# Optimization experiments

Hardware: AMD Instinct MI355X
Metric: run time of the kernel (lower is better)

Reference implementation:

```python
import jax, jax.numpy as jnp
import numpy as np

VOCAB_SIZE = 250002
UNUSED_TOKEN_IDS = np.array([0, 2, 1, 3])  # cls, eos, pad, unk (XLM-R tokenizer)
EPS = 1e-12


def _l2norm(x):
    n = jnp.sqrt(jnp.sum(x * x, axis=-1, keepdims=True))
    return x / jnp.maximum(n, EPS)


def setup_inputs() -> dict:
    key = jax.random.key(0)
    k1, k2, k3, k4 = jax.random.split(key, 4)
    B, S, H = 16, 2048, 1024
    hidden_state = jax.random.normal(k1, (B, S, H), dtype=jnp.float32)
    attention_mask = jnp.ones((B, S), dtype=jnp.float32)
    input_ids = jax.random.randint(k2, (B, S), 0, VOCAB_SIZE, dtype=jnp.int64)
    sparse_W = jax.random.normal(k3, (H, 1), dtype=jnp.float32) * 0.02
    sparse_b = jnp.zeros((1,), dtype=jnp.float32)
    colbert_W = jax.random.normal(k4, (H, H), dtype=jnp.float32) * 0.02
    colbert_b = jnp.zeros((H,), dtype=jnp.float32)
    return {
        "hidden_state": hidden_state,
        "attention_mask": attention_mask,
        "input_ids": input_ids,
        "sparse_W": sparse_W,
        "sparse_b": sparse_b,
        "colbert_W": colbert_W,
        "colbert_b": colbert_b,
    }


def reference(hidden_state, attention_mask, input_ids, sparse_W, sparse_b, colbert_W, colbert_b):
    B, S, H = hidden_state.shape
    # dense vector: CLS token, L2-normalized
    dense_vecs = _l2norm(hidden_state[:, 0])  # (B, H)

    # sparse: relu(Linear(H,1)) per token, scatter into vocab, max over seq.
    # scatter into zeros(B,S,V) + max over dim=1 == per-batch scatter-max into (B,V)
    token_weights = jax.nn.relu(
        jnp.einsum("bsh,ho->bso", hidden_state, sparse_W) + sparse_b
    )[..., 0]  # (B, S)
    batch_idx = jnp.arange(B)[:, None]  # (B, 1)
    sparse_vecs = jnp.zeros((B, VOCAB_SIZE), dtype=token_weights.dtype)
    sparse_vecs = sparse_vecs.at[batch_idx, input_ids].max(token_weights)
    # zero out special tokens (cls/eos/pad/unk)
    sparse_vecs = sparse_vecs.at[:, jnp.asarray(UNUSED_TOKEN_IDS)].set(0.0)

    # colbert: Linear(H,H) on tokens 1:, masked, then L2-normalized
    colbert_vecs = jnp.einsum("bsh,hd->bsd", hidden_state[:, 1:], colbert_W) + colbert_b
    colbert_vecs = colbert_vecs * attention_mask[:, 1:, None]
    colbert_vecs = _l2norm(colbert_vecs)  # (B, S-1, H)

    return dense_vecs, sparse_vecs, colbert_vecs
```

## Files before the change

kernel.cpp:

```cpp
#include <hip/hip_runtime.h>

#define HDIM 1024
#define SEQ  2048
#define BATCH 16
#define VOCAB 250002
#define M_TOT (BATCH * SEQ)
#define SPARSE_OFF (BATCH * HDIM)
#define COLBERT_OFF (SPARSE_OFF + BATCH * VOCAB)

typedef __attribute__((ext_vector_type(8))) short short8;
typedef __attribute__((ext_vector_type(4))) float f32x4;

static __device__ __forceinline__ unsigned short f2bf(float f) {
  union { float f; unsigned u; } v; v.f = f;
  unsigned r = v.u + 0x7fffu + ((v.u >> 16) & 1u);
  return (unsigned short)(r >> 16);
}

__global__ __launch_bounds__(256) void prep_kernel(
    const float* __restrict__ W, unsigned short* __restrict__ Wt,
    float* __restrict__ out, const float* __restrict__ hidden)
{
  __shared__ float tile[32][33];
  __shared__ float red[4];
  const int blk = blockIdx.x;
  if (blk < 1024) {
    const int n0 = (blk & 31) * 32, k0 = (blk >> 5) * 32;
    const int tx = threadIdx.x & 31, ty = threadIdx.x >> 5;
#pragma unroll
    for (int i = ty; i < 32; i += 8)
      tile[i][tx] = W[(size_t)(k0 + i) * HDIM + n0 + tx];
    __syncthreads();
#pragma unroll
    for (int i = ty; i < 32; i += 8) {
      const int n = n0 + i, k = k0 + tx;
      const size_t idx = (size_t)((n >> 4) * 32 + (k >> 5)) * 512
                       + (size_t)((((k >> 3) & 3) * 16 + (n & 15)) * 8 + (k & 7));
      Wt[idx] = f2bf(tile[tx][i]);
    }
  } else if (blk < 1536) {
    float4 z = {0.f, 0.f, 0.f, 0.f};
    float4* p = (float4*)(out + SPARSE_OFF);
    int idx = (blk - 1024) * 256 + threadIdx.x;
#pragma unroll 1
    for (; idx < 1000008; idx += 512 * 256) p[idx] = z;
  } else {
    const int b = blk - 1536;
    const int t = threadIdx.x;
    const float4* x = (const float4*)(hidden + (size_t)b * SEQ * HDIM);
    float4 v = x[t];
    float ss = v.x * v.x + v.y * v.y + v.z * v.z + v.w * v.w;
#pragma unroll
    for (int off = 32; off; off >>= 1) ss += __shfl_down(ss, off);
    if ((t & 63) == 0) red[t >> 6] = ss;
    __syncthreads();
    float tot = red[0] + red[1] + red[2] + red[3];
    float inv = 1.0f / fmaxf(sqrtf(tot), 1e-12f);
    v.x *= inv; v.y *= inv; v.z *= inv; v.w *= inv;
    ((float4*)(out + (size_t)b * HDIM))[t] = v;
  }
}

#define FUSED_LDS (64 * HDIM * 2 + (64 * 8 + 64) * 4)

__global__ __launch_bounds__(512, 2) void fused_kernel(
    const float* __restrict__ hidden,
    const unsigned short* __restrict__ Bp,
    const float* __restrict__ bias,
    const float* __restrict__ mask,
    const float* __restrict__ sparse_W,
    const float* __restrict__ sparse_b,
    const int* __restrict__ input_ids,
    float* __restrict__ out)
{
  extern __shared__ __align__(16) char smem[];
  unsigned short* As = (unsigned short*)smem;
  float* redLDS = (float*)(smem + 64 * HDIM * 2);
  float* invLDS = redLDS + 64 * 8;

  const int t = threadIdx.x;
  const int w = t >> 6, l = t & 63;
  const int q = l >> 4, ml = l & 15;
  const int mBase = blockIdx.x * 64;

  {
    const float sb = sparse_b[0];
    for (int r8 = 0; r8 < 8; r8++) {
      const int row = w * 8 + r8;
      const int gm = mBase + row;
      const float* src = hidden + (size_t)gm * HDIM;
      float dot = 0.f;
#pragma unroll
      for (int c = 0; c < 2; c++) {
        const int k0 = c * 512 + l * 8;
        f32x4 x0 = __builtin_nontemporal_load((const f32x4*)(src + k0));
        f32x4 x1 = __builtin_nontemporal_load((const f32x4*)(src + k0) + 1);
        const f32x4 w0 = *((const f32x4*)(sparse_W + k0));
        const f32x4 w1 = *((const f32x4*)(sparse_W + k0) + 1);
        dot = fmaf(x0.x, w0.x, dot); dot = fmaf(x0.y, w0.y, dot);
        dot = fmaf(x0.z, w0.z, dot); dot = fmaf(x0.w, w0.w, dot);
        dot = fmaf(x1.x, w1.x, dot); dot = fmaf(x1.y, w1.y, dot);
        dot = fmaf(x1.z, w1.z, dot); dot = fmaf(x1.w, w1.w, dot);
        short8 o;
        o[0] = (short)f2bf(x0.x); o[1] = (short)f2bf(x0.y);
        o[2] = (short)f2bf(x0.z); o[3] = (short)f2bf(x0.w);
        o[4] = (short)f2bf(x1.x); o[5] = (short)f2bf(x1.y);
        o[6] = (short)f2bf(x1.z); o[7] = (short)f2bf(x1.w);
        const int kk = k0 >> 5;
        const int slot = (((k0 >> 3) & 3) + (row >> 1)) & 3;
        const int byte = (kk * 4096 + row * 64 + slot * 16) ^ ((kk & 1) << 6);
        *(short8*)(smem + byte) = o;
      }
#pragma unroll
      for (int off = 32; off; off >>= 1) dot += __shfl_down(dot, off);
      if (l == 0) {
        const float wgt = dot + sb;
        if (wgt > 0.f) {
          const int id = input_ids[gm];
          if (id > 3) {
            const int b = gm >> 11;
            atomicMax((int*)(out + SPARSE_OFF + (size_t)b * VOCAB + id),
                      __float_as_int(wgt));
          }
        }
      }
    }
  }
  __syncthreads();

  int aoff[4];
#pragma unroll
  for (int i = 0; i < 4; i++) {
    const int ar = i * 16 + ml;
    aoff[i] = ar * 64 + (((q + (ar >> 1)) & 3) * 16);
  }
  const unsigned short* Bpw = Bp + (size_t)(w * 8 * 32) * 512 + l * 8;

  f32x4 acc[4][8] = {};
  short8 aC[4], aN[4], b0[4], b1[4];

#define LOADA(dst, KK) do {                                              \
    const int fl_ = ((KK) & 1) << 6;                                     \
    const int kb_ = (KK) * 4096;                                         \
    _Pragma("unroll")                                                    \
    for (int i_ = 0; i_ < 4; i_++)                                       \
      dst[i_] = *(const short8*)(smem + ((aoff[i_] ^ fl_) + kb_));       \
  } while (0)

#define LOADB(dst, JOFS, KK) do {                                        \
    _Pragma("unroll")                                                    \
    for (int j_ = 0; j_ < 4; j_++)                                       \
      dst[j_] = *(const short8*)(Bpw +                                   \
          (size_t)(((j_ + (JOFS)) * 32 + (KK)) * 512));                  \
  } while (0)

#define MF(AF, BF, JB) do {                                              \
    _Pragma("unroll")                                                    \
    for (int i_ = 0; i_ < 4; i_++)                                       \
      _Pragma("unroll")                                                  \
      for (int j_ = 0; j_ < 4; j_++)                                     \
        acc[i_][(JB) + j_] = __builtin_amdgcn_mfma_f32_16x16x32_bf16(    \
            AF[i_], BF[j_], acc[i_][(JB) + j_], 0, 0, 0);                \
  } while (0)

  LOADA(aC, 0);
  LOADB(b0, 0, 0);

#pragma unroll 1
  for (int kk = 0; kk < 32; kk += 2) {
    LOADB(b1, 4, kk);
    LOADA(aN, kk + 1);
    MF(aC, b0, 0);
    LOADB(b0, 0, kk + 1);
    MF(aC, b1, 4);
    const int k2 = (kk + 2) & 31;
    LOADB(b1, 4, kk + 1);
    LOADA(aC, k2);
    MF(aN, b0, 0);
    LOADB(b0, 0, k2);
    MF(aN, b1, 4);
  }

  float bv[8];
#pragma unroll
  for (int j = 0; j < 8; j++) bv[j] = bias[w * 128 + j * 16 + ml];
#pragma unroll
  for (int i = 0; i < 4; i++)
#pragma unroll
    for (int j = 0; j < 8; j++)
#pragma unroll
      for (int r = 0; r < 4; r++) acc[i][j][r] += bv[j];

#pragma unroll
  for (int i = 0; i < 4; i++) {
#pragma unroll
    for (int r = 0; r < 4; r++) {
      float ss = 0.0f;
#pragma unroll
      for (int j = 0; j < 8; j++) { float x = acc[i][j][r]; ss = fmaf(x, x, ss); }
      ss += __shfl_xor(ss, 1); ss += __shfl_xor(ss, 2);
      ss += __shfl_xor(ss, 4); ss += __shfl_xor(ss, 8);
      if (ml == 0) redLDS[(i * 16 + q * 4 + r) * 8 + w] = ss;
    }
  }
  __syncthreads();

  {
    const int row = t >> 3, wp = t & 7;
    float v = redLDS[row * 8 + wp];
    v += __shfl_xor(v, 1); v += __shfl_xor(v, 2); v += __shfl_xor(v, 4);
    if (wp == 0) {
      const int gm = mBase + row;
      const int s = gm & (SEQ - 1), b = gm >> 11;
      const float mval = mask[b * SEQ + s];
      invLDS[row] = mval / fmaxf(fabsf(mval) * sqrtf(v), 1e-12f);
    }
  }
  __syncthreads();

#pragma unroll
  for (int i = 0; i < 4; i++) {
#pragma unroll
    for (int r = 0; r < 4; r++) {
      const int row = i * 16 + q * 4 + r;
      const int gm = mBase + row;
      const int s = gm & (SEQ - 1);
      if (s != 0) {
        const int b = gm >> 11;
        float* orow = out + COLBERT_OFF + (size_t)(b * (SEQ - 1) + s - 1) * HDIM;
        const float iv = invLDS[row];
#pragma unroll
        for (int j = 0; j < 8; j++)
          __builtin_nontemporal_store(acc[i][j][r] * iv,
                                      orow + w * 128 + j * 16 + ml);
      }
    }
  }
}

extern "C" void kernel_launch(void* const* d_in, const int* in_sizes, int n_in,
                              void* d_out, int out_size, void* d_ws, size_t ws_size,
                              hipStream_t stream) {
  (void)in_sizes; (void)n_in; (void)out_size; (void)ws_size;
  const float* hidden = (const float*)d_in[0];
  const float* attn_mask = (const float*)d_in[1];
  const int* input_ids = (const int*)d_in[2];
  const float* sparse_W = (const float*)d_in[3];
  const float* sparse_b = (const float*)d_in[4];
  const float* colbert_W = (const float*)d_in[5];
  const float* colbert_b = (const float*)d_in[6];
  float* out = (float*)d_out;

  unsigned short* Wt = (unsigned short*)d_ws;

  prep_kernel<<<1552, 256, 0, stream>>>(colbert_W, Wt, out, hidden);
  fused_kernel<<<M_TOT / 64, 512, FUSED_LDS, stream>>>(
      hidden, Wt, colbert_b, attn_mask, sparse_W, sparse_b, input_ids, out);
}
```

Baseline: 335.8 us.

## Use 128-row tiles with double-buffered streamed A and two N-passes

Each block now covers 128 rows instead of 64. Rather than staging the whole bf16 row tile in LDS up front, A is streamed in 64-wide k chunks through a double-buffered LDS ring, with a prefetch of the next chunk overlapping the MFMAs. Output columns are split into two 512-wide passes that reread hidden. The first pass writes unnormalized results to global memory, and those are later reloaded and rescaled once the full row norm is known. This adds reuse of the B operand and overlap of loads with compute, at the cost of reading hidden twice and an extra read-modify-write of half the colbert output.

New measurement: 557.3 us. +66.0%, slower.

```diff
diff --git a/kernel.cpp b/kernel.cpp
--- a/kernel.cpp
+++ b/kernel.cpp
@@ -61,7 +61,9 @@
   }
 }
 
-#define FUSED_LDS (64 * HDIM * 2 + (64 * 8 + 64) * 4)
+#define ABUF_BYTES (128 * 64 * 2)
+#define RED_OFF    (2 * ABUF_BYTES)
+#define FUSED_LDS  (RED_OFF + (128 * 8 + 128 + 128) * 4)
 
 __global__ __launch_bounds__(512, 2) void fused_kernel(
     const float* __restrict__ hidden,
@@ -74,165 +76,245 @@
     float* __restrict__ out)
 {
   extern __shared__ __align__(16) char smem[];
-  unsigned short* As = (unsigned short*)smem;
-  float* redLDS = (float*)(smem + 64 * HDIM * 2);
-  float* invLDS = redLDS + 64 * 8;
+  float* redLDS = (float*)(smem + RED_OFF);
+  float* ssLDS  = redLDS + 128 * 8;
+  float* invLDS = ssLDS + 128;
 
   const int t = threadIdx.x;
   const int w = t >> 6, l = t & 63;
   const int q = l >> 4, ml = l & 15;
-  const int mBase = blockIdx.x * 64;
-
+  const int mBase = blockIdx.x * 128;
+
+  const int srow = t >> 2;
+  const int sseg = t & 3;
+  const float* srcRow = hidden + (size_t)(mBase + srow) * HDIM + sseg * 16;
+  const float* swRow  = sparse_W + sseg * 16;
+  int wb0, wb1;
   {
-    const float sb = sparse_b[0];
-    for (int r8 = 0; r8 < 8; r8++) {
-      const int row = w * 8 + r8;
-      const int gm = mBase + row;
-      const float* src = hidden + (size_t)gm * HDIM;
-      float dot = 0.f;
-#pragma unroll
-      for (int c = 0; c < 2; c++) {
-        const int k0 = c * 512 + l * 8;
-        f32x4 x0 = __builtin_nontemporal_load((const f32x4*)(src + k0));
-        f32x4 x1 = __builtin_nontemporal_load((const f32x4*)(src + k0) + 1);
-        const f32x4 w0 = *((const f32x4*)(sparse_W + k0));
-        const f32x4 w1 = *((const f32x4*)(sparse_W + k0) + 1);
-        dot = fmaf(x0.x, w0.x, dot); dot = fmaf(x0.y, w0.y, dot);
-        dot = fmaf(x0.z, w0.z, dot); dot = fmaf(x0.w, w0.w, dot);
-        dot = fmaf(x1.x, w1.x, dot); dot = fmaf(x1.y, w1.y, dot);
-        dot = fmaf(x1.z, w1.z, dot); dot = fmaf(x1.w, w1.w, dot);
-        short8 o;
-        o[0] = (short)f2bf(x0.x); o[1] = (short)f2bf(x0.y);
-        o[2] = (short)f2bf(x0.z); o[3] = (short)f2bf(x0.w);
-        o[4] = (short)f2bf(x1.x); o[5] = (short)f2bf(x1.y);
-        o[6] = (short)f2bf(x1.z); o[7] = (short)f2bf(x1.w);
-        const int kk = k0 >> 5;
-        const int slot = (((k0 >> 3) & 3) + (row >> 1)) & 3;
-        const int byte = (kk * 4096 + row * 64 + slot * 16) ^ ((kk & 1) << 6);
-        *(short8*)(smem + byte) = o;
-      }
-#pragma unroll
-      for (int off = 32; off; off >>= 1) dot += __shfl_down(dot, off);
-      if (l == 0) {
-        const float wgt = dot + sb;
-        if (wgt > 0.f) {
-          const int id = input_ids[gm];
-          if (id > 3) {
-            const int b = gm >> 11;
-            atomicMax((int*)(out + SPARSE_OFF + (size_t)b * VOCAB + id),
-                      __float_as_int(wgt));
-          }
-        }
-      }
-    }
+    const int ks0 = sseg * 2, ks1 = ks0 + 1;
+    wb0 = srow * 128 + ((((ks0 & 3) * 16) ^ ((srow & 3) << 4))
+        + (((ks0 >> 2) ^ ((srow >> 2) & 1)) << 6));
+    wb1 = srow * 128 + ((((ks1 & 3) * 16) ^ ((srow & 3) << 4))
+        + (((ks1 >> 2) ^ ((srow >> 2) & 1)) << 6));
   }
-  __syncthreads();
-
-  int aoff[4];
-#pragma unroll
-  for (int i = 0; i < 4; i++) {
-    const int ar = i * 16 + ml;
-    aoff[i] = ar * 64 + (((q + (ar >> 1)) & 3) * 16);
+
+  int aoff0[8];
+#pragma unroll
+  for (int i = 0; i < 8; i++) {
+    const int row = i * 16 + ml;
+    aoff0[i] = row * 128 + (((q * 16) ^ ((row & 3) << 4)) + (((row >> 2) & 1) << 6));
   }
-  const unsigned short* Bpw = Bp + (size_t)(w * 8 * 32) * 512 + l * 8;
-
-  f32x4 acc[4][8] = {};
-  short8 aC[4], aN[4], b0[4], b1[4];
-
-#define LOADA(dst, KK) do {                                              \
-    const int fl_ = ((KK) & 1) << 6;                                     \
-    const int kb_ = (KK) * 4096;                                         \
+
+  float dot = 0.f;
+  f32x4 sx[4];
+  f32x4 acc[8][4];
+  short8 af[8], bC[4], bN[4];
+#pragma unroll
+  for (int i = 0; i < 8; i++)
+#pragma unroll
+    for (int j = 0; j < 4; j++) acc[i][j] = (f32x4){0.f, 0.f, 0.f, 0.f};
+
+#define SLOAD(KC) do {                                                   \
     _Pragma("unroll")                                                    \
-    for (int i_ = 0; i_ < 4; i_++)                                       \
-      dst[i_] = *(const short8*)(smem + ((aoff[i_] ^ fl_) + kb_));       \
-  } while (0)
-
-#define LOADB(dst, JOFS, KK) do {                                        \
+    for (int h_ = 0; h_ < 4; h_++)                                       \
+      sx[h_] = *(const f32x4*)(srcRow + (KC) * 64 + h_ * 4);             \
+  } while (0)
+
+#define SWRITE(BUFOFS, KC, DODOT) do {                                   \
+    if (DODOT) {                                                         \
+      _Pragma("unroll")                                                  \
+      for (int h_ = 0; h_ < 4; h_++) {                                   \
+        const f32x4 wv_ = *(const f32x4*)(swRow + (KC) * 64 + h_ * 4);   \
+        dot = fmaf(sx[h_].x, wv_.x, dot); dot = fmaf(sx[h_].y, wv_.y, dot); \
+        dot = fmaf(sx[h_].z, wv_.z, dot); dot = fmaf(sx[h_].w, wv_.w, dot); \
+      }                                                                  \
+    }                                                                    \
+    short8 o0_, o1_;                                                     \
+    o0_[0] = (short)f2bf(sx[0].x); o0_[1] = (short)f2bf(sx[0].y);        \
+    o0_[2] = (short)f2bf(sx[0].z); o0_[3] = (short)f2bf(sx[0].w);        \
+    o0_[4] = (short)f2bf(sx[1].x); o0_[5] = (short)f2bf(sx[1].y);        \
+    o0_[6] = (short)f2bf(sx[1].z); o0_[7] = (short)f2bf(sx[1].w);        \
+    o1_[0] = (short)f2bf(sx[2].x); o1_[1] = (short)f2bf(sx[2].y);        \
+    o1_[2] = (short)f2bf(sx[2].z); o1_[3] = (short)f2bf(sx[2].w);        \
+    o1_[4] = (short)f2bf(sx[3].x); o1_[5] = (short)f2bf(sx[3].y);        \
+    o1_[6] = (short)f2bf(sx[3].z); o1_[7] = (short)f2bf(sx[3].w);        \
+    *(short8*)(smem + (BUFOFS) + wb0) = o0_;                             \
+    *(short8*)(smem + (BUFOFS) + wb1) = o1_;                             \
+  } while (0)
+
+#define LOADA(BUFOFS, KK2) do {                                          \
+    _Pragma("unroll")                                                    \
+    for (int i_ = 0; i_ < 8; i_++)                                       \
+      af[i_] = *(const short8*)(smem + (BUFOFS) + (aoff0[i_] ^ ((KK2) << 6))); \
+  } while (0)
+
+#define LOADB(DST, K32) do {                                             \
     _Pragma("unroll")                                                    \
     for (int j_ = 0; j_ < 4; j_++)                                       \
-      dst[j_] = *(const short8*)(Bpw +                                   \
-          (size_t)(((j_ + (JOFS)) * 32 + (KK)) * 512));                  \
-  } while (0)
-
-#define MF(AF, BF, JB) do {                                              \
+      DST[j_] = *(const short8*)(Bpw + (size_t)((j_ * 32 + (K32)) * 512)); \
+  } while (0)
+
+#define MF(BF) do {                                                      \
     _Pragma("unroll")                                                    \
-    for (int i_ = 0; i_ < 4; i_++)                                       \
+    for (int i_ = 0; i_ < 8; i_++)                                       \
       _Pragma("unroll")                                                  \
       for (int j_ = 0; j_ < 4; j_++)                                     \
-        acc[i_][(JB) + j_] = __builtin_amdgcn_mfma_f32_16x16x32_bf16(    \
-            AF[i_], BF[j_], acc[i_][(JB) + j_], 0, 0, 0);                \
-  } while (0)
-
-  LOADA(aC, 0);
-  LOADB(b0, 0, 0);
+        acc[i_][j_] = __builtin_amdgcn_mfma_f32_16x16x32_bf16(           \
+            af[i_], BF[j_], acc[i_][j_], 0, 0, 0);                       \
+  } while (0)
 
 #pragma unroll 1
-  for (int kk = 0; kk < 32; kk += 2) {
-    LOADB(b1, 4, kk);
-    LOADA(aN, kk + 1);
-    MF(aC, b0, 0);
-    LOADB(b0, 0, kk + 1);
-    MF(aC, b1, 4);
-    const int k2 = (kk + 2) & 31;
-    LOADB(b1, 4, kk + 1);
-    LOADA(aC, k2);
-    MF(aN, b0, 0);
-    LOADB(b0, 0, k2);
-    MF(aN, b1, 4);
-  }
-
-  float bv[8];
-#pragma unroll
-  for (int j = 0; j < 8; j++) bv[j] = bias[w * 128 + j * 16 + ml];
-#pragma unroll
-  for (int i = 0; i < 4; i++)
-#pragma unroll
-    for (int j = 0; j < 8; j++)
-#pragma unroll
-      for (int r = 0; r < 4; r++) acc[i][j][r] += bv[j];
-
-#pragma unroll
-  for (int i = 0; i < 4; i++) {
-#pragma unroll
-    for (int r = 0; r < 4; r++) {
-      float ss = 0.0f;
-#pragma unroll
-      for (int j = 0; j < 8; j++) { float x = acc[i][j][r]; ss = fmaf(x, x, ss); }
-      ss += __shfl_xor(ss, 1); ss += __shfl_xor(ss, 2);
-      ss += __shfl_xor(ss, 4); ss += __shfl_xor(ss, 8);
-      if (ml == 0) redLDS[(i * 16 + q * 4 + r) * 8 + w] = ss;
+  for (int pass = 0; pass < 2; pass++) {
+    const unsigned short* Bpw =
+        Bp + ((size_t)(pass * 32 + w * 4) * 32) * 512 + l * 8;
+
+    SLOAD(0);
+    SWRITE(0, 0, pass == 0);
+    LOADB(bC, 0);
+    __syncthreads();
+
+#pragma unroll 1
+    for (int kc = 0; kc < 16; kc++) {
+      const int bufofs = (kc & 1) * ABUF_BYTES;
+      if (kc < 15) SLOAD(kc + 1);
+      LOADB(bN, kc * 2 + 1);
+      LOADA(bufofs, 0);
+      MF(bC);
+      LOADB(bC, (kc * 2 + 2) & 31);
+      LOADA(bufofs, 1);
+      MF(bN);
+      if (kc < 15) {
+        SWRITE(((kc + 1) & 1) * ABUF_BYTES, kc + 1, pass == 0);
+        __syncthreads();
+      }
     }
-  }
-  __syncthreads();
-
-  {
-    const int row = t >> 3, wp = t & 7;
-    float v = redLDS[row * 8 + wp];
-    v += __shfl_xor(v, 1); v += __shfl_xor(v, 2); v += __shfl_xor(v, 4);
-    if (wp == 0) {
-      const int gm = mBase + row;
-      const int s = gm & (SEQ - 1), b = gm >> 11;
-      const float mval = mask[b * SEQ + s];
-      invLDS[row] = mval / fmaxf(fabsf(mval) * sqrtf(v), 1e-12f);
-    }
-  }
-  __syncthreads();
-
-#pragma unroll
-  for (int i = 0; i < 4; i++) {
-#pragma unroll
-    for (int r = 0; r < 4; r++) {
-      const int row = i * 16 + q * 4 + r;
-      const int gm = mBase + row;
-      const int s = gm & (SEQ - 1);
-      if (s != 0) {
-        const int b = gm >> 11;
-        float* orow = out + COLBERT_OFF + (size_t)(b * (SEQ - 1) + s - 1) * HDIM;
-        const float iv = invLDS[row];
-#pragma unroll
-        for (int j = 0; j < 8; j++)
-          __builtin_nontemporal_store(acc[i][j][r] * iv,
-                                      orow + w * 128 + j * 16 + ml);
+
+    if (pass == 0) {
+      float bv[4];
+#pragma unroll
+      for (int j = 0; j < 4; j++) bv[j] = bias[w * 64 + j * 16 + ml];
+#pragma unroll
+      for (int i = 0; i < 8; i++) {
+#pragma unroll
+        for (int r = 0; r < 4; r++) {
+          float ss = 0.f;
+#pragma unroll
+          for (int j = 0; j < 4; j++) {
+            acc[i][j][r] += bv[j];
+            const float x = acc[i][j][r];
+            ss = fmaf(x, x, ss);
+          }
+          ss += __shfl_xor(ss, 1); ss += __shfl_xor(ss, 2);
+          ss += __shfl_xor(ss, 4); ss += __shfl_xor(ss, 8);
+          if (ml == 0) redLDS[(i * 16 + q * 4 + r) * 8 + w] = ss;
+        }
+      }
+      __syncthreads();
+      if (t < 128) {
+        float v = 0.f;
+#pragma unroll
+        for (int p = 0; p < 8; p++) v += redLDS[t * 8 + p];
+        ssLDS[t] = v;
+      }
+#pragma unroll
+      for (int i = 0; i < 8; i++) {
+#pragma unroll
+        for (int r = 0; r < 4; r++) {
+          const int row = i * 16 + q * 4 + r;
+          const int gm = mBase + row;
+          const int s = gm & (SEQ - 1);
+          if (s != 0) {
+            const int b = gm >> 11;
+            float* orow = out + COLBERT_OFF + (size_t)(b * (SEQ - 1) + s - 1) * HDIM;
+#pragma unroll
+            for (int j = 0; j < 4; j++)
+              orow[w * 64 + j * 16 + ml] = acc[i][j][r];
+          }
+        }
+      }
+      {
+        float d = dot;
+        d += __shfl_xor(d, 1); d += __shfl_xor(d, 2);
+        if (sseg == 0) {
+          const float wgt = d + sparse_b[0];
+          if (wgt > 0.f) {
+            const int gm = mBase + srow;
+            const int id = input_ids[gm];
+            if (id > 3) {
+              atomicMax((int*)(out + SPARSE_OFF + (size_t)(gm >> 11) * VOCAB + id),
+                        __float_as_int(wgt));
+            }
+          }
+        }
+      }
+#pragma unroll
+      for (int i = 0; i < 8; i++)
+#pragma unroll
+        for (int j = 0; j < 4; j++) acc[i][j] = (f32x4){0.f, 0.f, 0.f, 0.f};
+      __syncthreads();
+    } else {
+      float bv[4];
+#pragma unroll
+      for (int j = 0; j < 4; j++) bv[j] = bias[512 + w * 64 + j * 16 + ml];
+#pragma unroll
+      for (int i = 0; i < 8; i++) {
+#pragma unroll
+        for (int r = 0; r < 4; r++) {
+          float ss = 0.f;
+#pragma unroll
+          for (int j = 0; j < 4; j++) {
+            acc[i][j][r] += bv[j];
+            const float x = acc[i][j][r];
+            ss = fmaf(x, x, ss);
+          }
+          ss += __shfl_xor(ss, 1); ss += __shfl_xor(ss, 2);
+          ss += __shfl_xor(ss, 4); ss += __shfl_xor(ss, 8);
+          if (ml == 0) redLDS[(i * 16 + q * 4 + r) * 8 + w] = ss;
+        }
+      }
+      __syncthreads();
+      if (t < 128) {
+        float v = ssLDS[t];
+#pragma unroll
+        for (int p = 0; p < 8; p++) v += redLDS[t * 8 + p];
+        const int gm = mBase + t;
+        const int s = gm & (SEQ - 1), b = gm >> 11;
+        const float mval = mask[b * SEQ + s];
+        invLDS[t] = mval / fmaxf(fabsf(mval) * sqrtf(v), 1e-12f);
+      }
+      __syncthreads();
+#pragma unroll
+      for (int i = 0; i < 8; i++) {
+#pragma unroll
+        for (int r = 0; r < 4; r++) {
+          const int row = i * 16 + q * 4 + r;
+          const int gm = mBase + row;
+          const int s = gm & (SEQ - 1);
+          if (s != 0) {
+            const int b = gm >> 11;
+            float* orow = out + COLBERT_OFF + (size_t)(b * (SEQ - 1) + s - 1) * HDIM;
+            const float iv = invLDS[row];
+#pragma unroll
+            for (int j = 0; j < 4; j++)
+              orow[512 + w * 64 + j * 16 + ml] = acc[i][j][r] * iv;
+          }
+        }
+      }
+#pragma unroll 1
+      for (int k2 = 0; k2 < 32; k2++) {
+        const int idx = k2 * 512 + t;
+        const int row = idx >> 7, c4 = idx & 127;
+        const int gm = mBase + row;
+        const int s = gm & (SEQ - 1);
+        if (s != 0) {
+          const int b = gm >> 11;
+          f32x4* p = (f32x4*)(out + COLBERT_OFF +
+                              (size_t)(b * (SEQ - 1) + s - 1) * HDIM) + c4;
+          const float iv = invLDS[row];
+          f32x4 vv = *p;
+          vv.x *= iv; vv.y *= iv; vv.z *= iv; vv.w *= iv;
+          *p = vv;
+        }
       }
     }
   }
@@ -254,6 +336,6 @@
   unsigned short* Wt = (unsigned short*)d_ws;
 
   prep_kernel<<<1552, 256, 0, stream>>>(colbert_W, Wt, out, hidden);
-  fused_kernel<<<M_TOT / 64, 512, FUSED_LDS, stream>>>(
+  fused_kernel<<<M_TOT / 128, 512, FUSED_LDS, stream>>>(
       hidden, Wt, colbert_b, attn_mask, sparse_W, sparse_b, input_ids, out);
 }
```
